# Optimization experiments

Hardware: AMD Instinct MI355X
Metric: run time of the kernel (lower is better)

Reference implementation:

```python
import jax, jax.numpy as jnp
import numpy as np

IOU_THRESHOLD = 0.1
EPS = 1e-7  # torchvision generalized_box_iou_loss eps


def _make_boxes(key, b, n, img=1000.0, wmin=10.0, wmax=120.0):
    k1, k2 = jax.random.split(key)
    cxy = jax.random.uniform(k1, (b, n, 2), jnp.float32, 0.0, img)
    wh = jax.random.uniform(k2, (b, n, 2), jnp.float32, wmin, wmax)
    return jnp.concatenate([cxy - 0.5 * wh, cxy + 0.5 * wh], axis=-1)  # xyxy


def setup_inputs() -> dict:
    key = jax.random.key(0)
    kp, kt = jax.random.split(key)
    pred_boxes = _make_boxes(kp, 16, 4096)    # [B, M, 4]
    target_boxes = _make_boxes(kt, 16, 512)   # [B, N, 4]
    return {"pred_boxes": pred_boxes, "target_boxes": target_boxes}


def _pairwise_iou(p, t):
    # p: [M,4], t: [N,4] xyxy -> [M,N]
    area_p = (p[:, 2] - p[:, 0]) * (p[:, 3] - p[:, 1])
    area_t = (t[:, 2] - t[:, 0]) * (t[:, 3] - t[:, 1])
    lt = jnp.maximum(p[:, None, :2], t[None, :, :2])
    rb = jnp.minimum(p[:, None, 2:], t[None, :, 2:])
    wh = jnp.clip(rb - lt, 0.0)
    inter = wh[..., 0] * wh[..., 1]
    union = area_p[:, None] + area_t[None, :] - inter
    return inter / union


def _greedy_match(iou):
    # Greedy: for each pred row (in order), take highest-IoU unused target with IoU > thr.
    N = iou.shape[1]
    def step(used, row):
        masked = jnp.where(used, -jnp.inf, row)  # [N]
        j = jnp.argmax(masked)
        valid = masked[j] > IOU_THRESHOLD
        used = used.at[j].set(used[j] | valid)
        return used, (j, valid)
    _, (idx, valid) = jax.lax.scan(step, jnp.zeros((N,), bool), iou)
    return idx, valid  # [M] int, [M] bool


def _giou_loss_pairs(p, t):
    # elementwise GIoU loss between p[i] and t[i]; p,t: [K,4] -> [K]
    x1 = jnp.maximum(p[:, 0], t[:, 0]); y1 = jnp.maximum(p[:, 1], t[:, 1])
    x2 = jnp.minimum(p[:, 2], t[:, 2]); y2 = jnp.minimum(p[:, 3], t[:, 3])
    inter = jnp.clip(x2 - x1, 0.0) * jnp.clip(y2 - y1, 0.0)
    area_p = (p[:, 2] - p[:, 0]) * (p[:, 3] - p[:, 1])
    area_t = (t[:, 2] - t[:, 0]) * (t[:, 3] - t[:, 1])
    union = area_p + area_t - inter
    iou = inter / (union + EPS)
    ex1 = jnp.minimum(p[:, 0], t[:, 0]); ey1 = jnp.minimum(p[:, 1], t[:, 1])
    ex2 = jnp.maximum(p[:, 2], t[:, 2]); ey2 = jnp.maximum(p[:, 3], t[:, 3])
    enc = (ex2 - ex1) * (ey2 - ey1)
    giou = iou - (enc - union) / (enc + EPS)
    return 1.0 - giou


def _image_loss(pred, tgt):
    # pred [M,4], tgt [N,4] with M != N -> greedy match then mean GIoU loss over matches
    iou = _pairwise_iou(pred, tgt)
    idx, valid = _greedy_match(iou)
    matched_t = tgt[idx]                    # [M,4]
    loss = _giou_loss_pairs(pred, matched_t)
    w = valid.astype(loss.dtype)
    cnt = w.sum()
    return jnp.where(cnt > 0, (loss * w).sum() / jnp.maximum(cnt, 1.0), 0.0)


def reference(pred_boxes, target_boxes):
    # batched path, reduction='mean': mean over per-image mean GIoU losses
    per_image = jax.vmap(_image_loss)(pred_boxes, target_boxes)  # [B]
    return per_image.mean()
```

## Files before the change

kernel.cpp:

```cpp
#include <hip/hip_runtime.h>
#include <math.h>

#define NB   16
#define NM   4096
#define NT   512
#define CAP  16
#define IOU_THR 0.1f
#define EPSG 1e-7f
#define NROWS (NB*NM)
#define T_WIN 1024
#define NWIN  (NM / T_WIN)
#define SENT  0xFFFFFFFFu

__global__ __launch_bounds__(256) void cand_kernel(
    const float4* __restrict__ pred, const float4* __restrict__ tgt,
    int* __restrict__ counts, float2* __restrict__ cands, int* __restrict__ done_ctr)
{
    __shared__ float4 t_lds[NT];
    const int rb = blockIdx.x * 32;
    const int b  = rb >> 12;
    if (blockIdx.x == 0 && threadIdx.x == 0) *done_ctr = 0;
    #pragma unroll
    for (int i = 0; i < 2; ++i)
        t_lds[i * 256 + threadIdx.x] = tgt[b * NT + i * 256 + threadIdx.x];
    __syncthreads();

    const int wv = threadIdx.x >> 6, lane = threadIdx.x & 63;
    const int row0 = rb + wv * 8;
    const unsigned long long lmask = (1ull << lane) - 1ull;

    float4 pn0 = pred[row0],     pn1 = pred[row0 + 1];
    float4 pn2 = pred[row0 + 2], pn3 = pred[row0 + 3];
    for (int rr = 0; rr < 8; rr += 4) {
        float4 p0 = pn0, p1 = pn1, p2 = pn2, p3 = pn3;
        if (rr + 4 < 8) {
            pn0 = pred[row0 + rr + 4]; pn1 = pred[row0 + rr + 5];
            pn2 = pred[row0 + rr + 6]; pn3 = pred[row0 + rr + 7];
        }
        float ap0 = (p0.z - p0.x) * (p0.w - p0.y);
        float ap1 = (p1.z - p1.x) * (p1.w - p1.y);
        float ap2 = (p2.z - p2.x) * (p2.w - p2.y);
        float ap3 = (p3.z - p3.x) * (p3.w - p3.y);
        int base0 = 0, base1 = 0, base2 = 0, base3 = 0;
        #pragma unroll
        for (int pass = 0; pass < NT / 64; ++pass) {
            int j = (pass << 6) + lane;
            float4 t = t_lds[j];
            float at = (t.z - t.x) * (t.w - t.y);
            float w0 = fmaxf(fminf(p0.z, t.z) - fmaxf(p0.x, t.x), 0.f);
            float h0 = fmaxf(fminf(p0.w, t.w) - fmaxf(p0.y, t.y), 0.f);
            float in0 = w0 * h0;
            float iou0 = in0 * __builtin_amdgcn_rcpf((ap0 + at) - in0);
            float w1 = fmaxf(fminf(p1.z, t.z) - fmaxf(p1.x, t.x), 0.f);
            float h1 = fmaxf(fminf(p1.w, t.w) - fmaxf(p1.y, t.y), 0.f);
            float in1 = w1 * h1;
            float iou1 = in1 * __builtin_amdgcn_rcpf((ap1 + at) - in1);
            float w2 = fmaxf(fminf(p2.z, t.z) - fmaxf(p2.x, t.x), 0.f);
            float h2 = fmaxf(fminf(p2.w, t.w) - fmaxf(p2.y, t.y), 0.f);
            float in2 = w2 * h2;
            float iou2 = in2 * __builtin_amdgcn_rcpf((ap2 + at) - in2);
            float w3 = fmaxf(fminf(p3.z, t.z) - fmaxf(p3.x, t.x), 0.f);
            float h3 = fmaxf(fminf(p3.w, t.w) - fmaxf(p3.y, t.y), 0.f);
            float in3 = w3 * h3;
            float iou3 = in3 * __builtin_amdgcn_rcpf((ap3 + at) - in3);
            bool q0 = iou0 > IOU_THR, q1 = iou1 > IOU_THR;
            bool q2 = iou2 > IOU_THR, q3 = iou3 > IOU_THR;
            unsigned long long m0 = __ballot(q0), m1 = __ballot(q1);
            unsigned long long m2 = __ballot(q2), m3 = __ballot(q3);
            if (q0) {
                int off = base0 + __popcll(m0 & lmask);
                if (off < CAP)
                    cands[(size_t)off * NROWS + row0 + rr]     = make_float2(iou0, __int_as_float(j));
            }
            if (q1) {
                int off = base1 + __popcll(m1 & lmask);
                if (off < CAP)
                    cands[(size_t)off * NROWS + row0 + rr + 1] = make_float2(iou1, __int_as_float(j));
            }
            if (q2) {
                int off = base2 + __popcll(m2 & lmask);
                if (off < CAP)
                    cands[(size_t)off * NROWS + row0 + rr + 2] = make_float2(iou2, __int_as_float(j));
            }
            if (q3) {
                int off = base3 + __popcll(m3 & lmask);
                if (off < CAP)
                    cands[(size_t)off * NROWS + row0 + rr + 3] = make_float2(iou3, __int_as_float(j));
            }
            base0 += __popcll(m0); base1 += __popcll(m1);
            base2 += __popcll(m2); base3 += __popcll(m3);
        }
        if (lane == 0) {
            counts[row0 + rr]     = base0;
            counts[row0 + rr + 1] = base1;
            counts[row0 + rr + 2] = base2;
            counts[row0 + rr + 3] = base3;
        }
    }
}

__global__ __launch_bounds__(T_WIN) void win_auction(
    const float4* __restrict__ pred, const float4* __restrict__ tgt,
    const int* __restrict__ counts, const float2* __restrict__ cands,
    float* __restrict__ per_img, int* __restrict__ done_ctr,
    float* __restrict__ out)
{
    __shared__ float4   t_lds[NT];
    __shared__ unsigned claim[NT];
    __shared__ int lastprop;
    __shared__ unsigned char winovf[NWIN];
    __shared__ int ovf_min, ovf_res;
    __shared__ float rvv[T_WIN / 64];  __shared__ int rjj[T_WIN / 64];
    __shared__ float rls[T_WIN / 64];  __shared__ float rcs[T_WIN / 64];

    const int b = blockIdx.x, t = threadIdx.x, gbase = b * NM;
    const int wv = t >> 6, lane = t & 63;

    if (t < NT) {
        t_lds[t] = tgt[b * NT + t];
        claim[t] = SENT;
    }
    if (t < NWIN) winovf[t] = 0;
    if (t == 0) lastprop = -1;
    __syncthreads();

    int allCnt[NWIN];
    #pragma unroll
    for (int k = 0; k < NWIN; ++k) {
        allCnt[k] = counts[gbase + k * T_WIN + t];
        if (allCnt[k] > CAP) winovf[k] = 1;
    }
    float2 nC[CAP];
    #pragma unroll
    for (int e = 0; e < CAP; ++e) nC[e] = cands[(size_t)e * NROWS + gbase + t];
    __syncthreads();

    int rglob = 0;
    float2 cC[CAP];
    for (int w = 0; w < NWIN; ++w) {
        #pragma unroll
        for (int e = 0; e < CAP; ++e) cC[e] = nC[e];
        const int cCnt = allCnt[w];
        if (w + 1 < NWIN) {
            #pragma unroll
            for (int e = 0; e < CAP; ++e)
                nC[e] = cands[(size_t)e * NROWS + gbase + (w + 1) * T_WIN + t];
        }
        const unsigned row = (unsigned)(w * T_WIN + t);
        int  stt  = (cCnt > 0 && cCnt <= CAP) ? 0 : 2;
        int  myj  = -1;
        bool isovf = (cCnt > CAP);
        int  ovfj  = -1;

        for (;;) {
            for (;;) {
                if (stt == 1 && claim[myj] != row) stt = 0;
                bool did = false;
                if (stt == 0) {
                    for (int it = 0; it <= CAP; ++it) {
                        float bv = -1.f; int bj = -1;
                        #pragma unroll
                        for (int e = 0; e < CAP; ++e) {
                            float2 ce = cC[e];
                            int j = __float_as_int(ce.y) & (NT - 1);
                            unsigned cj = claim[j];
                            if (e < cCnt && cj >= row && ce.x > bv) { bv = ce.x; bj = j; }
                        }
                        if (bj < 0) { stt = 2; break; }
                        did = true;
                        unsigned old = atomicMin(&claim[bj], row);
                        if (old >= row) { myj = bj; stt = 1; break; }
                    }
                }
                if (did) lastprop = rglob;
                __syncthreads();
                int lp = lastprop;
                ++rglob;
                if (lp < rglob - 1) break;
            }
            if (!winovf[w]) break;
            if (t == 0) ovf_min = 0x7FFFFFFF;
            __syncthreads();
            bool pend = isovf && (ovfj < 0 || claim[ovfj] != row);
            if (pend) atomicMin(&ovf_min, (int)row);
            __syncthreads();
            const int rowF = ovf_min;
            if (rowF == 0x7FFFFFFF) break;
            {
                float4 p4 = pred[gbase + rowF];
                float v = -1.f; int bj = NT;
                if (t < NT) {
                    float4 tt = t_lds[t];
                    float area_p = (p4.z - p4.x) * (p4.w - p4.y);
                    float area_t = (tt.z - tt.x) * (tt.w - tt.y);
                    float wd = fmaxf(fminf(p4.z, tt.z) - fmaxf(p4.x, tt.x), 0.f);
                    float hd = fmaxf(fminf(p4.w, tt.w) - fmaxf(p4.y, tt.y), 0.f);
                    float inter = wd * hd;
                    float iou = inter / ((area_p + area_t) - inter);
                    bool freej = claim[t] > (unsigned)rowF;
                    v = freej ? iou : -1.f;
                    bj = freej ? t : NT;
                }
                #pragma unroll
                for (int off = 1; off < 64; off <<= 1) {
                    float ov = __shfl_xor(v, off);
                    int   oj = __shfl_xor(bj, off);
                    if (ov > v || (ov == v && oj < bj)) { v = ov; bj = oj; }
                }
                if (lane == 0) { rvv[wv] = v; rjj[wv] = bj; }
            }
            __syncthreads();
            if (t == 0) {
                float v = rvv[0]; int bj = rjj[0];
                for (int q = 1; q < T_WIN / 64; ++q)
                    if (rvv[q] > v || (rvv[q] == v && rjj[q] < bj)) { v = rvv[q]; bj = rjj[q]; }
                if (v > IOU_THR) { ovf_res = bj; claim[bj] = (unsigned)rowF; }
                else ovf_res = -1;
            }
            __syncthreads();
            if ((int)row == rowF) {
                if (ovf_res >= 0) ovfj = ovf_res;
                else isovf = false;
            }
        }
    }
    __syncthreads();

    float ls = 0.f, cs = 0.f;
    if (t < NT) {
        unsigned r = claim[t];
        if (r != SENT) {
            float4 p4 = pred[gbase + (int)r];
            float4 tt = t_lds[t];
            float inter = fmaxf(fminf(p4.z, tt.z) - fmaxf(p4.x, tt.x), 0.f) *
                          fmaxf(fminf(p4.w, tt.w) - fmaxf(p4.y, tt.y), 0.f);
            float area_p = (p4.z - p4.x) * (p4.w - p4.y);
            float area_t = (tt.z - tt.x) * (tt.w - tt.y);
            float uni = area_p + area_t - inter;
            float iou = inter / (uni + EPSG);
            float enc = (fmaxf(p4.z, tt.z) - fminf(p4.x, tt.x)) *
                        (fmaxf(p4.w, tt.w) - fminf(p4.y, tt.y));
            float giou = iou - (enc - uni) / (enc + EPSG);
            ls = 1.f - giou;
            cs = 1.f;
        }
    }
    #pragma unroll
    for (int off = 32; off >= 1; off >>= 1) {
        ls += __shfl_xor(ls, off);
        cs += __shfl_xor(cs, off);
    }
    if (lane == 0) { rls[wv] = ls; rcs[wv] = cs; }
    __syncthreads();
    if (t == 0) {
        float L = 0.f, C = 0.f;
        for (int q = 0; q < T_WIN / 64; ++q) { L += rls[q]; C += rcs[q]; }
        per_img[b] = (C > 0.f) ? L / C : 0.f;
        __threadfence();
        int ret = atomicAdd(done_ctr, 1);
        if (ret == NB - 1) {
            __threadfence();
            volatile float* vp = per_img;
            float s = 0.f;
            for (int i = 0; i < NB; ++i) s += vp[i];
            out[0] = s / (float)NB;
        }
    }
}

extern "C" void kernel_launch(void* const* d_in, const int* in_sizes, int n_in,
                              void* d_out, int out_size, void* d_ws, size_t ws_size,
                              hipStream_t stream)
{
    const float4* pred = (const float4*)d_in[0];
    const float4* tgt  = (const float4*)d_in[1];

    char* ws = (char*)d_ws;
    int*    counts  = (int*)ws;
    size_t  off1    = (size_t)NROWS * sizeof(int);
    float2* cands   = (float2*)(ws + off1);
    size_t  off2    = off1 + (size_t)CAP * NROWS * sizeof(float2);
    float*  per_img = (float*)(ws + off2);
    int*    done_ctr = (int*)(ws + off2 + 64);

    cand_kernel<<<NROWS / 32, 256, 0, stream>>>(pred, tgt, counts, cands, done_ctr);
    win_auction<<<NB, T_WIN, 0, stream>>>(pred, tgt, counts, cands, per_img,
                                          done_ctr, (float*)d_out);
}
```

Before: 56.32 us.

## Process two rows per thread to halve greedy-match window count

Each thread of the 1024-thread matching block now owns two pred rows per window, so the window spans 2048 rows and only two windows are needed instead of four. The intent is to halve the number of block-wide synchronisation rounds of the iterative claim/resolve loop. The cost is doubled candidate registers per thread (two CAP-sized arrays), loss of the next-window prefetch, and possibly more propagation rounds per window because more rows contend at once.

Result: faster. 54.38 us, median of 2 (-3.4%).

```diff
diff --git a/kernel.cpp b/kernel.cpp
--- a/kernel.cpp
+++ b/kernel.cpp
@@ -9,7 +9,8 @@
 #define EPSG 1e-7f
 #define NROWS (NB*NM)
 #define T_WIN 1024
-#define NWIN  (NM / T_WIN)
+#define WROWS 2048
+#define NWIN  (NM / WROWS)
 #define SENT  0xFFFFFFFFu
 
 __global__ __launch_bounds__(256) void cand_kernel(
@@ -124,52 +125,69 @@
     if (t == 0) lastprop = -1;
     __syncthreads();
 
-    int allCnt[NWIN];
-    #pragma unroll
-    for (int k = 0; k < NWIN; ++k) {
-        allCnt[k] = counts[gbase + k * T_WIN + t];
-        if (allCnt[k] > CAP) winovf[k] = 1;
-    }
-    float2 nC[CAP];
-    #pragma unroll
-    for (int e = 0; e < CAP; ++e) nC[e] = cands[(size_t)e * NROWS + gbase + t];
+    int cw00, cw01, cw10, cw11;
+    cw00 = counts[gbase + 0 * WROWS + t];
+    cw01 = counts[gbase + 0 * WROWS + T_WIN + t];
+    cw10 = counts[gbase + 1 * WROWS + t];
+    cw11 = counts[gbase + 1 * WROWS + T_WIN + t];
+    if (cw00 > CAP || cw01 > CAP) winovf[0] = 1;
+    if (cw10 > CAP || cw11 > CAP) winovf[1] = 1;
     __syncthreads();
 
     int rglob = 0;
-    float2 cC[CAP];
+    #pragma unroll 1
     for (int w = 0; w < NWIN; ++w) {
+        float2 c0[CAP], c1[CAP];
         #pragma unroll
-        for (int e = 0; e < CAP; ++e) cC[e] = nC[e];
-        const int cCnt = allCnt[w];
-        if (w + 1 < NWIN) {
-            #pragma unroll
-            for (int e = 0; e < CAP; ++e)
-                nC[e] = cands[(size_t)e * NROWS + gbase + (w + 1) * T_WIN + t];
-        }
-        const unsigned row = (unsigned)(w * T_WIN + t);
-        int  stt  = (cCnt > 0 && cCnt <= CAP) ? 0 : 2;
-        int  myj  = -1;
-        bool isovf = (cCnt > CAP);
-        int  ovfj  = -1;
+        for (int e = 0; e < CAP; ++e) {
+            c0[e] = cands[(size_t)e * NROWS + gbase + w * WROWS + t];
+            c1[e] = cands[(size_t)e * NROWS + gbase + w * WROWS + T_WIN + t];
+        }
+        const unsigned row0 = (unsigned)(w * WROWS + t);
+        const unsigned row1 = (unsigned)(w * WROWS + T_WIN + t);
+        const int cnt0 = (w == 0) ? cw00 : cw10;
+        const int cnt1 = (w == 0) ? cw01 : cw11;
+        int  stt0 = (cnt0 > 0 && cnt0 <= CAP) ? 0 : 2;
+        int  stt1 = (cnt1 > 0 && cnt1 <= CAP) ? 0 : 2;
+        int  myj0 = -1, myj1 = -1;
+        bool isovf0 = (cnt0 > CAP), isovf1 = (cnt1 > CAP);
+        int  ovfj0 = -1, ovfj1 = -1;
 
         for (;;) {
             for (;;) {
-                if (stt == 1 && claim[myj] != row) stt = 0;
                 bool did = false;
-                if (stt == 0) {
+                if (stt0 == 1 && claim[myj0] != row0) stt0 = 0;
+                if (stt0 == 0) {
                     for (int it = 0; it <= CAP; ++it) {
                         float bv = -1.f; int bj = -1;
                         #pragma unroll
                         for (int e = 0; e < CAP; ++e) {
-                            float2 ce = cC[e];
+                            float2 ce = c0[e];
                             int j = __float_as_int(ce.y) & (NT - 1);
                             unsigned cj = claim[j];
-                            if (e < cCnt && cj >= row && ce.x > bv) { bv = ce.x; bj = j; }
+                            if (e < cnt0 && cj >= row0 && ce.x > bv) { bv = ce.x; bj = j; }
                         }
-                        if (bj < 0) { stt = 2; break; }
+                        if (bj < 0) { stt0 = 2; break; }
                         did = true;
-                        unsigned old = atomicMin(&claim[bj], row);
-                        if (old >= row) { myj = bj; stt = 1; break; }
+                        unsigned old = atomicMin(&claim[bj], row0);
+                        if (old >= row0) { myj0 = bj; stt0 = 1; break; }
+                    }
+                }
+                if (stt1 == 1 && claim[myj1] != row1) stt1 = 0;
+                if (stt1 == 0) {
+                    for (int it = 0; it <= CAP; ++it) {
+                        float bv = -1.f; int bj = -1;
+                        #pragma unroll
+                        for (int e = 0; e < CAP; ++e) {
+                            float2 ce = c1[e];
+                            int j = __float_as_int(ce.y) & (NT - 1);
+                            unsigned cj = claim[j];
+                            if (e < cnt1 && cj >= row1 && ce.x > bv) { bv = ce.x; bj = j; }
+                        }
+                        if (bj < 0) { stt1 = 2; break; }
+                        did = true;
+                        unsigned old = atomicMin(&claim[bj], row1);
+                        if (old >= row1) { myj1 = bj; stt1 = 1; break; }
                     }
                 }
                 if (did) lastprop = rglob;
@@ -181,8 +199,10 @@
             if (!winovf[w]) break;
             if (t == 0) ovf_min = 0x7FFFFFFF;
             __syncthreads();
-            bool pend = isovf && (ovfj < 0 || claim[ovfj] != row);
-            if (pend) atomicMin(&ovf_min, (int)row);
+            bool pend0 = isovf0 && (ovfj0 < 0 || claim[ovfj0] != row0);
+            bool pend1 = isovf1 && (ovfj1 < 0 || claim[ovfj1] != row1);
+            if (pend0) atomicMin(&ovf_min, (int)row0);
+            if (pend1) atomicMin(&ovf_min, (int)row1);
             __syncthreads();
             const int rowF = ovf_min;
             if (rowF == 0x7FFFFFFF) break;
@@ -218,9 +238,13 @@
                 else ovf_res = -1;
             }
             __syncthreads();
-            if ((int)row == rowF) {
-                if (ovf_res >= 0) ovfj = ovf_res;
-                else isovf = false;
+            if ((int)row0 == rowF) {
+                if (ovf_res >= 0) ovfj0 = ovf_res;
+                else isovf0 = false;
+            }
+            if ((int)row1 == rowF) {
+                if (ovf_res >= 0) ovfj1 = ovf_res;
+                else isovf1 = false;
             }
         }
     }
```
